# Performance work log

Hardware: AMD Instinct MI355X
Metric: run time of the kernel (lower is better)

The kernel has to match this reference:

```python
import jax, jax.numpy as jnp
import numpy as np

B, C, L = 8, 512, 2048
D = C // 8  # qk projection dim


def setup_inputs() -> dict:
    key = jax.random.key(0)
    ks = jax.random.split(key, 7)
    s = 0.02
    return {
        "x": jax.random.normal(ks[0], (B, C, L), dtype=jnp.float32),
        "data_mask": jnp.zeros((B, L, L), dtype=bool),
        "Wq": jax.random.normal(ks[1], (D, C), dtype=jnp.float32) * s,
        "bq": jnp.zeros((D,), dtype=jnp.float32),
        "Wk": jax.random.normal(ks[2], (D, C), dtype=jnp.float32) * s,
        "bk": jnp.zeros((D,), dtype=jnp.float32),
        "Wv": jax.random.normal(ks[3], (C, C), dtype=jnp.float32) * s,
        "bv": jnp.zeros((C,), dtype=jnp.float32),
    }


def reference(x, data_mask, Wq, bq, Wk, bk, Wv, bv):
    # Conv1d(kernel_size=1) == pointwise linear over channel dim.
    Lx = x.shape[-1]
    q = jnp.einsum("dc,bcl->bld", Wq, x) + bq              # (B, L, D)  == query_conv(x).permute(0,2,1)
    k = jnp.einsum("dc,bcl->bdl", Wk, x) + bk[:, None]     # (B, D, L)
    energy = jnp.einsum("bld,bdm->blm", q, k)              # (B, L, L)
    causal = jnp.triu(jnp.ones((Lx, Lx), dtype=bool), k=1)  # strictly-upper = masked
    mask = causal[None, :, :] | data_mask
    energy = jnp.where(mask, -jnp.inf, energy)
    attention = jax.nn.softmax(energy, axis=-1)            # (B, L, L)
    v = jnp.einsum("oc,bcl->bol", Wv, x) + bv[:, None]     # (B, C, L)
    # out = bmm(proj_value, attention^T): out[b,c,m] = sum_l v[b,c,l] * attention[b,m,l]
    out = jnp.einsum("bcl,bml->bcm", v, attention)         # (B, C, L)
    return out, attention
```

## Files before the change

### kernel.cpp

```cpp
#include <hip/hip_runtime.h>
#include <cstddef>
#include <math.h>

#define B_ 8
#define C_ 512
#define L_ 2048
#define D_ 64

typedef __bf16 bf16x8 __attribute__((ext_vector_type(8)));
typedef __bf16 bf16x4 __attribute__((ext_vector_type(4)));
typedef float f32x4 __attribute__((ext_vector_type(4)));

#define MFMA16 __builtin_amdgcn_mfma_f32_16x16x32_bf16

__device__ __forceinline__ void async_lds16(const void* g, void* l) {
  __builtin_amdgcn_global_load_lds(
      (const __attribute__((address_space(1))) void*)g,
      (__attribute__((address_space(3))) void*)l, 16, 0, 0);
}

__global__ __launch_bounds__(256) void transpose_cvt(const float* __restrict__ x,
                                                     __bf16* __restrict__ xT) {
  __shared__ float t[32][33];
  const int b = blockIdx.z;
  const int l0 = blockIdx.x * 32, c0 = blockIdx.y * 32;
  const int tx = threadIdx.x & 31, ty = threadIdx.x >> 5;
  const float* xb = x + (size_t)b * C_ * L_;
#pragma unroll
  for (int r = 0; r < 4; ++r)
    t[ty + r * 8][tx] = xb[(size_t)(c0 + ty + r * 8) * L_ + l0 + tx];
  __syncthreads();
  __bf16* xTb = xT + (size_t)b * L_ * C_;
#pragma unroll
  for (int r = 0; r < 4; ++r)
    xTb[(size_t)(l0 + ty + r * 8) * C_ + c0 + tx] = (__bf16)t[tx][ty + r * 8];
}

__global__ __launch_bounds__(256) void cvt_bf16(const float* __restrict__ in,
                                                __bf16* __restrict__ out, int n4) {
  const int i = blockIdx.x * 256 + threadIdx.x;
  if (i < n4) {
    float4 v = ((const float4*)in)[i];
    bf16x4 h = {(__bf16)v.x, (__bf16)v.y, (__bf16)v.z, (__bf16)v.w};
    ((bf16x4*)out)[i] = h;
  }
}

__global__ __launch_bounds__(256) void prep_qk(
    const float* __restrict__ Wq, const float* __restrict__ Wk,
    const float* __restrict__ bq, const float* __restrict__ bk,
    __bf16* __restrict__ Wqk, float* __restrict__ bqk) {
  const int i = blockIdx.x * 256 + threadIdx.x;
  const int half = 64 * 512 / 4;
  const float* src = (i < half) ? Wq : Wk;
  const int j = (i < half) ? i : i - half;
  float4 v = ((const float4*)src)[j];
  bf16x4 h = {(__bf16)v.x, (__bf16)v.y, (__bf16)v.z, (__bf16)v.w};
  ((bf16x4*)Wqk)[i] = h;
  if (blockIdx.x == 0 && threadIdx.x < 128)
    bqk[threadIdx.x] =
        threadIdx.x < 64 ? bq[threadIdx.x] : bk[threadIdx.x - 64];
}

template <int QK_MODE>
__global__ __launch_bounds__(256) void gemm_bt_mfma(
    const __bf16* __restrict__ A, const __bf16* __restrict__ B,
    const float* __restrict__ bias, __bf16* __restrict__ C0,
    __bf16* __restrict__ C1, int N, int K, int lda, int ldb, size_t strideA,
    size_t strideB, size_t strideC) {
  __shared__ __align__(16) __bf16 Ash[128 * 32];
  __shared__ __align__(16) __bf16 Bsh[128 * 32];
  const int b = blockIdx.z;
  const int m0 = blockIdx.x * 128;
  const int n0 = blockIdx.y * 128;
  const int tid = threadIdx.x;
  const int w = tid >> 6, lane = tid & 63;
  const int wm = (w & 1) * 64, wn = (w >> 1) * 64;
  const int lm = lane & 15, q8 = lane >> 4;
  const int srow = lane >> 2;
  const int sk8 = (lane & 3) ^ ((lane >> 3) & 3);

  const __bf16* Ab = A + strideA * b;
  const __bf16* Bb = B + strideB * b;
  f32x4 acc[4][4] = {};

  for (int k0 = 0; k0 < K; k0 += 32) {
#pragma unroll
    for (int t = 0; t < 2; ++t) {
      const int rb = (t * 4 + w) * 16;
      async_lds16(Ab + (size_t)(m0 + rb + srow) * lda + k0 + sk8 * 8,
                  &Ash[rb * 32]);
      async_lds16(Bb + (size_t)(n0 + rb + srow) * ldb + k0 + sk8 * 8,
                  &Bsh[rb * 32]);
    }
    __syncthreads();
    const int swz = (q8 ^ ((lm >> 1) & 3)) * 8;
    bf16x8 afr[4], bfr[4];
#pragma unroll
    for (int i = 0; i < 4; ++i) {
      afr[i] = *(const bf16x8*)&Ash[(wm + i * 16 + lm) * 32 + swz];
      bfr[i] = *(const bf16x8*)&Bsh[(wn + i * 16 + lm) * 32 + swz];
    }
#pragma unroll
    for (int i = 0; i < 4; ++i)
#pragma unroll
      for (int j = 0; j < 4; ++j)
        acc[i][j] = MFMA16(afr[i], bfr[j], acc[i][j], 0, 0, 0);
    __syncthreads();
  }

#pragma unroll
  for (int i = 0; i < 4; ++i) {
#pragma unroll
    for (int j = 0; j < 4; ++j) {
      const int ng = n0 + wn + j * 16 + lm;
      const int mgb = wm + i * 16 + q8 * 4;
      if (QK_MODE) {
        bf16x4 h;
#pragma unroll
        for (int r = 0; r < 4; ++r) h[r] = (__bf16)(acc[i][j][r] + bias[mgb + r]);
        if (mgb < 64)
          *(bf16x4*)&C0[((size_t)b * L_ + ng) * 64 + mgb] = h;
        else
          *(bf16x4*)&C1[((size_t)b * L_ + ng) * 64 + mgb - 64] = h;
      } else {
#pragma unroll
        for (int r = 0; r < 4; ++r) {
          const int mg = m0 + mgb + r;
          C0[strideC * b + (size_t)mg * N + ng] =
              (__bf16)(acc[i][j][r] + bias[mg]);
        }
      }
    }
  }
}

__global__ __launch_bounds__(256) void attn_fused(
    const __bf16* __restrict__ q, const __bf16* __restrict__ k,
    const __bf16* __restrict__ v, const unsigned char* __restrict__ mask,
    float* __restrict__ att, float* __restrict__ out) {
  __shared__ __align__(16) __bf16 qs[32 * 64];
  __shared__ __align__(16) __bf16 ks[2][128 * 64];
  __shared__ __align__(16) unsigned char msk[2][32 * 128];
  __shared__ __align__(16) __bf16 Ps[32 * 136];
  __shared__ float sums[4][32];
  __shared__ float invs[32];
  const int b = blockIdx.y;
  const int s = (b < 4) ? (int)blockIdx.x : 63 - (int)blockIdx.x;
  const int r0 = s * 32;
  const int T = (r0 + 31) / 128 + 1;
  const int tid = threadIdx.x;
  const int w = tid >> 6, lane = tid & 63;
  const int lm = lane & 15, q8 = lane >> 4;
  const __bf16* qb = q + (size_t)b * L_ * D_;
  const __bf16* kb = k + (size_t)b * L_ * D_;
  const __bf16* vb = v + (size_t)b * C_ * L_;
  const int krow = lane >> 3;
  const int kk8 = (lane & 7) ^ ((lane >> 3) & 7);

  bf16x8 af[2][2];
  float inv[2][4];
  f32x4 accO[2][8] = {};

  for (int pass = 0; pass < 2; ++pass) {
    __syncthreads();
    if (pass == 0)
      async_lds16(qb + (size_t)r0 * D_ + tid * 8, &qs[w * 512]);
#pragma unroll
    for (int r = 0; r < 4; ++r)
      async_lds16(kb + (size_t)(r * 32 + w * 8 + krow) * 64 + kk8 * 8,
                  &ks[0][(r * 32 + w * 8) * 64]);
    async_lds16(mask + (size_t)((size_t)b * L_ + r0 + w * 8 + krow) * L_ +
                    (lane & 7) * 16,
                &msk[0][w * 1024]);

    float rsum[2][4] = {};
    for (int t = 0; t < T; ++t) {
      const int t0 = t * 128;
      const int buf = t & 1;
      __syncthreads();
      if (pass == 0 && t == 0) {
#pragma unroll
        for (int i = 0; i < 2; ++i)
#pragma unroll
          for (int kk = 0; kk < 2; ++kk)
            af[i][kk] =
                *(const bf16x8*)&qs[(i * 16 + lm) * 64 + kk * 32 + q8 * 8];
      }
      if (t + 1 < T) {
        const int nt0 = t0 + 128, nb = (t + 1) & 1;
#pragma unroll
        for (int r = 0; r < 4; ++r)
          async_lds16(kb + (size_t)(nt0 + r * 32 + w * 8 + krow) * 64 + kk8 * 8,
                      &ks[nb][(r * 32 + w * 8) * 64]);
        async_lds16(mask + (size_t)((size_t)b * L_ + r0 + w * 8 + krow) * L_ +
                        nt0 + (lane & 7) * 16,
                    &msk[nb][w * 1024]);
      }
      f32x4 acc[2][2] = {};
#pragma unroll
      for (int kk = 0; kk < 2; ++kk) {
#pragma unroll
        for (int j = 0; j < 2; ++j) {
          const int n = w * 32 + j * 16 + lm;
          const int k8i = kk * 4 + q8;
          bf16x8 bf =
              *(const bf16x8*)&ks[buf][n * 64 + ((k8i ^ (n & 7)) * 8)];
#pragma unroll
          for (int i = 0; i < 2; ++i)
            acc[i][j] = MFMA16(af[i][kk], bf, acc[i][j], 0, 0, 0);
        }
      }
#pragma unroll
      for (int i = 0; i < 2; ++i)
#pragma unroll
        for (int j = 0; j < 2; ++j)
#pragma unroll
          for (int r = 0; r < 4; ++r) {
            const int lr = i * 16 + q8 * 4 + r;
            const int mcol = w * 32 + j * 16 + lm;
            const int l = r0 + lr, m = t0 + mcol;
            const bool ok = (m <= l) && (msk[buf][lr * 128 + mcol] == 0);
            const float p = ok ? __expf(acc[i][j][r]) : 0.f;
            if (pass == 0) {
              rsum[i][r] += p;
            } else {
              att[((size_t)b * L_ + l) * L_ + m] = p * inv[i][r];
              Ps[lr * 136 + mcol] = (__bf16)p;
            }
          }
      if (pass == 1) {
        __syncthreads();
#pragma unroll
        for (int kk = 0; kk < 4; ++kk) {
          bf16x8 pa[2];
#pragma unroll
          for (int i = 0; i < 2; ++i)
            pa[i] = *(const bf16x8*)&Ps[(i * 16 + lm) * 136 + kk * 32 + q8 * 8];
#pragma unroll
          for (int cf = 0; cf < 8; ++cf) {
            const int c = w * 128 + cf * 16 + lm;
            bf16x8 bv =
                *(const bf16x8*)(vb + (size_t)c * L_ + t0 + kk * 32 + q8 * 8);
#pragma unroll
            for (int i = 0; i < 2; ++i)
              accO[i][cf] = MFMA16(pa[i], bv, accO[i][cf], 0, 0, 0);
          }
        }
      }
    }
    if (pass == 0) {
#pragma unroll
      for (int i = 0; i < 2; ++i)
#pragma unroll
        for (int r = 0; r < 4; ++r) {
          float vv = rsum[i][r];
          vv += __shfl_xor(vv, 1);
          vv += __shfl_xor(vv, 2);
          vv += __shfl_xor(vv, 4);
          vv += __shfl_xor(vv, 8);
          if (lm == 0) sums[w][i * 16 + q8 * 4 + r] = vv;
        }
      __syncthreads();
      if (tid < 32)
        invs[tid] =
            1.f / (sums[0][tid] + sums[1][tid] + sums[2][tid] + sums[3][tid]);
      __syncthreads();
#pragma unroll
      for (int i = 0; i < 2; ++i)
#pragma unroll
        for (int r = 0; r < 4; ++r) inv[i][r] = invs[i * 16 + q8 * 4 + r];
    }
  }

#pragma unroll
  for (int i = 0; i < 2; ++i)
#pragma unroll
    for (int cf = 0; cf < 8; ++cf) {
      const int c = w * 128 + cf * 16 + lm;
      float4 o;
      o.x = accO[i][cf][0] * inv[i][0];
      o.y = accO[i][cf][1] * inv[i][1];
      o.z = accO[i][cf][2] * inv[i][2];
      o.w = accO[i][cf][3] * inv[i][3];
      *(float4*)(out + ((size_t)b * C_ + c) * L_ + r0 + i * 16 + q8 * 4) = o;
    }

  const float4 z4 = {0.f, 0.f, 0.f, 0.f};
  for (int rr = 0; rr < 32; ++rr) {
    float* arow = att + ((size_t)b * L_ + r0 + rr) * L_;
    for (int c = T * 128 + tid * 4; c < L_; c += 1024) *(float4*)&arow[c] = z4;
  }
}

extern "C" void kernel_launch(void* const* d_in, const int* in_sizes, int n_in,
                              void* d_out, int out_size, void* d_ws,
                              size_t ws_size, hipStream_t stream) {
  const float* x = (const float*)d_in[0];
  const unsigned char* dmask = (const unsigned char*)d_in[1];
  const float* Wq = (const float*)d_in[2];
  const float* bq = (const float*)d_in[3];
  const float* Wk = (const float*)d_in[4];
  const float* bk = (const float*)d_in[5];
  const float* Wv = (const float*)d_in[6];
  const float* bv = (const float*)d_in[7];

  float* out = (float*)d_out;
  float* att = out + (size_t)B_ * C_ * L_;

  __bf16* qh = (__bf16*)d_ws;
  __bf16* kh = qh + (size_t)B_ * L_ * D_;
  __bf16* xTh = kh + (size_t)B_ * L_ * D_;
  __bf16* Wvh = xTh + (size_t)B_ * L_ * C_;
  __bf16* vh = Wvh + (size_t)C_ * C_;
  __bf16* Wqk = vh + (size_t)B_ * C_ * L_;
  float* bqk = (float*)(Wqk + (size_t)128 * C_);

  dim3 blk(256);
  transpose_cvt<<<dim3(L_ / 32, C_ / 32, B_), blk, 0, stream>>>(x, xTh);
  cvt_bf16<<<dim3(C_ * C_ / 4 / 256), blk, 0, stream>>>(Wv, Wvh, C_ * C_ / 4);
  prep_qk<<<dim3(64), blk, 0, stream>>>(Wq, Wk, bq, bk, Wqk, bqk);
  gemm_bt_mfma<1><<<dim3(1, L_ / 128, B_), blk, 0, stream>>>(
      Wqk, xTh, bqk, qh, kh, L_, C_, C_, C_, 0, (size_t)L_ * C_, 0);
  gemm_bt_mfma<0><<<dim3(C_ / 128, L_ / 128, B_), blk, 0, stream>>>(
      Wvh, xTh, bv, vh, nullptr, L_, C_, C_, C_, 0, (size_t)L_ * C_,
      (size_t)C_ * L_);
  attn_fused<<<dim3(64, B_), blk, 0, stream>>>(qh, kh, vh, dmask, att, out);
}
```

Measured before the change: 417.4 us.

## Split softmax row-sum pass into separate kernel and fuse QKV projection GEMMs

The row-sum pass of the two-pass softmax moves out of the attention kernel into its own row_sums kernel, which writes inverse sums to workspace reused from the xT buffer. The attention kernel then does a single pass that writes attention and accumulates P·V. The Q/K and V weight conversions and GEMMs are also merged into one prep kernel and one 5-row-block GEMM launch, cutting launch count and letting the QK and V work share a grid. The extra kernel reloads Q/K/mask and adds a global round trip for the sums, but the attention kernel's per-block serial work is roughly halved.

```diff
diff --git a/kernel.cpp b/kernel.cpp
--- a/kernel.cpp
+++ b/kernel.cpp
@@ -36,38 +36,36 @@
     xTb[(size_t)(l0 + ty + r * 8) * C_ + c0 + tx] = (__bf16)t[tx][ty + r * 8];
 }
 
-__global__ __launch_bounds__(256) void cvt_bf16(const float* __restrict__ in,
-                                                __bf16* __restrict__ out, int n4) {
+__global__ __launch_bounds__(256) void prep_qkv(
+    const float* __restrict__ Wq, const float* __restrict__ Wk,
+    const float* __restrict__ Wv, const float* __restrict__ bq,
+    const float* __restrict__ bk, const float* __restrict__ bv,
+    __bf16* __restrict__ W, float* __restrict__ bias) {
   const int i = blockIdx.x * 256 + threadIdx.x;
-  if (i < n4) {
-    float4 v = ((const float4*)in)[i];
-    bf16x4 h = {(__bf16)v.x, (__bf16)v.y, (__bf16)v.z, (__bf16)v.w};
-    ((bf16x4*)out)[i] = h;
-  }
-}
-
-__global__ __launch_bounds__(256) void prep_qk(
-    const float* __restrict__ Wq, const float* __restrict__ Wk,
-    const float* __restrict__ bq, const float* __restrict__ bk,
-    __bf16* __restrict__ Wqk, float* __restrict__ bqk) {
-  const int i = blockIdx.x * 256 + threadIdx.x;
-  const int half = 64 * 512 / 4;
-  const float* src = (i < half) ? Wq : Wk;
-  const int j = (i < half) ? i : i - half;
+  const int rq = 64 * 512 / 4;
+  const int rk = 128 * 512 / 4;
+  const float* src;
+  int j;
+  if (i < rq) {
+    src = Wq; j = i;
+  } else if (i < rk) {
+    src = Wk; j = i - rq;
+  } else {
+    src = Wv; j = i - rk;
+  }
   float4 v = ((const float4*)src)[j];
   bf16x4 h = {(__bf16)v.x, (__bf16)v.y, (__bf16)v.z, (__bf16)v.w};
-  ((bf16x4*)Wqk)[i] = h;
-  if (blockIdx.x == 0 && threadIdx.x < 128)
-    bqk[threadIdx.x] =
-        threadIdx.x < 64 ? bq[threadIdx.x] : bk[threadIdx.x - 64];
-}
-
-template <int QK_MODE>
-__global__ __launch_bounds__(256) void gemm_bt_mfma(
-    const __bf16* __restrict__ A, const __bf16* __restrict__ B,
-    const float* __restrict__ bias, __bf16* __restrict__ C0,
-    __bf16* __restrict__ C1, int N, int K, int lda, int ldb, size_t strideA,
-    size_t strideB, size_t strideC) {
+  ((bf16x4*)W)[i] = h;
+  if (blockIdx.x == 0) {
+    for (int t = threadIdx.x; t < 640; t += 256)
+      bias[t] = t < 64 ? bq[t] : (t < 128 ? bk[t - 64] : bv[t - 128]);
+  }
+}
+
+__global__ __launch_bounds__(256) void gemm_qkv(
+    const __bf16* __restrict__ A, const __bf16* __restrict__ Bm,
+    const float* __restrict__ bias, __bf16* __restrict__ qh,
+    __bf16* __restrict__ kh, __bf16* __restrict__ vh) {
   __shared__ __align__(16) __bf16 Ash[128 * 32];
   __shared__ __align__(16) __bf16 Bsh[128 * 32];
   const int b = blockIdx.z;
@@ -80,17 +78,16 @@
   const int srow = lane >> 2;
   const int sk8 = (lane & 3) ^ ((lane >> 3) & 3);
 
-  const __bf16* Ab = A + strideA * b;
-  const __bf16* Bb = B + strideB * b;
+  const __bf16* Bb = Bm + (size_t)b * L_ * C_;
   f32x4 acc[4][4] = {};
 
-  for (int k0 = 0; k0 < K; k0 += 32) {
+  for (int k0 = 0; k0 < C_; k0 += 32) {
 #pragma unroll
     for (int t = 0; t < 2; ++t) {
       const int rb = (t * 4 + w) * 16;
-      async_lds16(Ab + (size_t)(m0 + rb + srow) * lda + k0 + sk8 * 8,
+      async_lds16(A + (size_t)(m0 + rb + srow) * C_ + k0 + sk8 * 8,
                   &Ash[rb * 32]);
-      async_lds16(Bb + (size_t)(n0 + rb + srow) * ldb + k0 + sk8 * 8,
+      async_lds16(Bb + (size_t)(n0 + rb + srow) * C_ + k0 + sk8 * 8,
                   &Bsh[rb * 32]);
     }
     __syncthreads();
@@ -114,37 +111,126 @@
 #pragma unroll
     for (int j = 0; j < 4; ++j) {
       const int ng = n0 + wn + j * 16 + lm;
-      const int mgb = wm + i * 16 + q8 * 4;
-      if (QK_MODE) {
+      const int mg = m0 + wm + i * 16 + q8 * 4;
+      if (mg < 128) {
         bf16x4 h;
 #pragma unroll
-        for (int r = 0; r < 4; ++r) h[r] = (__bf16)(acc[i][j][r] + bias[mgb + r]);
-        if (mgb < 64)
-          *(bf16x4*)&C0[((size_t)b * L_ + ng) * 64 + mgb] = h;
+        for (int r = 0; r < 4; ++r) h[r] = (__bf16)(acc[i][j][r] + bias[mg + r]);
+        if (mg < 64)
+          *(bf16x4*)&qh[((size_t)b * L_ + ng) * 64 + mg] = h;
         else
-          *(bf16x4*)&C1[((size_t)b * L_ + ng) * 64 + mgb - 64] = h;
+          *(bf16x4*)&kh[((size_t)b * L_ + ng) * 64 + mg - 64] = h;
       } else {
 #pragma unroll
+        for (int r = 0; r < 4; ++r)
+          vh[((size_t)b * C_ + mg - 128 + r) * L_ + ng] =
+              (__bf16)(acc[i][j][r] + bias[mg + r]);
+      }
+    }
+  }
+}
+
+__global__ __launch_bounds__(256) void row_sums(
+    const __bf16* __restrict__ q, const __bf16* __restrict__ k,
+    const unsigned char* __restrict__ mask, float* __restrict__ sinv) {
+  __shared__ __align__(16) __bf16 qs[32 * 64];
+  __shared__ __align__(16) __bf16 ks[2][128 * 64];
+  __shared__ __align__(16) unsigned char msk[2][32 * 128];
+  __shared__ float sums[4][32];
+  const int b = blockIdx.y;
+  const int s = (b < 4) ? (int)blockIdx.x : 63 - (int)blockIdx.x;
+  const int r0 = s * 32;
+  const int T = (r0 + 31) / 128 + 1;
+  const int tid = threadIdx.x;
+  const int w = tid >> 6, lane = tid & 63;
+  const int lm = lane & 15, q8 = lane >> 4;
+  const __bf16* qb = q + (size_t)b * L_ * D_;
+  const __bf16* kb = k + (size_t)b * L_ * D_;
+  const int krow = lane >> 3;
+  const int kk8 = (lane & 7) ^ ((lane >> 3) & 7);
+
+  async_lds16(qb + (size_t)r0 * D_ + tid * 8, &qs[w * 512]);
+#pragma unroll
+  for (int r = 0; r < 4; ++r)
+    async_lds16(kb + (size_t)(r * 32 + w * 8 + krow) * 64 + kk8 * 8,
+                &ks[0][(r * 32 + w * 8) * 64]);
+  async_lds16(mask + ((size_t)b * L_ + r0 + w * 8 + krow) * L_ + (lane & 7) * 16,
+              &msk[0][w * 1024]);
+
+  bf16x8 af[2][2];
+  float rsum[2][4] = {};
+  for (int t = 0; t < T; ++t) {
+    const int t0 = t * 128, buf = t & 1;
+    __syncthreads();
+    if (t == 0) {
+#pragma unroll
+      for (int i = 0; i < 2; ++i)
+#pragma unroll
+        for (int kk = 0; kk < 2; ++kk)
+          af[i][kk] = *(const bf16x8*)&qs[(i * 16 + lm) * 64 + kk * 32 + q8 * 8];
+    }
+    if (t + 1 < T) {
+      const int nt0 = t0 + 128, nb = (t + 1) & 1;
+#pragma unroll
+      for (int r = 0; r < 4; ++r)
+        async_lds16(kb + (size_t)(nt0 + r * 32 + w * 8 + krow) * 64 + kk8 * 8,
+                    &ks[nb][(r * 32 + w * 8) * 64]);
+      async_lds16(mask + ((size_t)b * L_ + r0 + w * 8 + krow) * L_ + nt0 +
+                      (lane & 7) * 16,
+                  &msk[nb][w * 1024]);
+    }
+    f32x4 acc[2][2] = {};
+#pragma unroll
+    for (int kk = 0; kk < 2; ++kk) {
+#pragma unroll
+      for (int j = 0; j < 2; ++j) {
+        const int n = w * 32 + j * 16 + lm;
+        const int k8i = kk * 4 + q8;
+        bf16x8 bf = *(const bf16x8*)&ks[buf][n * 64 + ((k8i ^ (n & 7)) * 8)];
+#pragma unroll
+        for (int i = 0; i < 2; ++i)
+          acc[i][j] = MFMA16(af[i][kk], bf, acc[i][j], 0, 0, 0);
+      }
+    }
+#pragma unroll
+    for (int i = 0; i < 2; ++i)
+#pragma unroll
+      for (int j = 0; j < 2; ++j)
+#pragma unroll
         for (int r = 0; r < 4; ++r) {
-          const int mg = m0 + mgb + r;
-          C0[strideC * b + (size_t)mg * N + ng] =
-              (__bf16)(acc[i][j][r] + bias[mg]);
+          const int lr = i * 16 + q8 * 4 + r;
+          const int mcol = w * 32 + j * 16 + lm;
+          const int l = r0 + lr, m = t0 + mcol;
+          const bool ok = (m <= l) && (msk[buf][lr * 128 + mcol] == 0);
+          rsum[i][r] += ok ? __expf(acc[i][j][r]) : 0.f;
         }
-      }
-    }
-  }
+  }
+#pragma unroll
+  for (int i = 0; i < 2; ++i)
+#pragma unroll
+    for (int r = 0; r < 4; ++r) {
+      float vv = rsum[i][r];
+      vv += __shfl_xor(vv, 1);
+      vv += __shfl_xor(vv, 2);
+      vv += __shfl_xor(vv, 4);
+      vv += __shfl_xor(vv, 8);
+      if (lm == 0) sums[w][i * 16 + q8 * 4 + r] = vv;
+    }
+  __syncthreads();
+  if (tid < 32)
+    sinv[(size_t)b * L_ + r0 + tid] =
+        1.f / (sums[0][tid] + sums[1][tid] + sums[2][tid] + sums[3][tid]);
 }
 
 __global__ __launch_bounds__(256) void attn_fused(
     const __bf16* __restrict__ q, const __bf16* __restrict__ k,
     const __bf16* __restrict__ v, const unsigned char* __restrict__ mask,
-    float* __restrict__ att, float* __restrict__ out) {
+    const float* __restrict__ sinv, float* __restrict__ att,
+    float* __restrict__ out) {
   __shared__ __align__(16) __bf16 qs[32 * 64];
   __shared__ __align__(16) __bf16 ks[2][128 * 64];
   __shared__ __align__(16) unsigned char msk[2][32 * 128];
   __shared__ __align__(16) __bf16 Ps[32 * 136];
-  __shared__ float sums[4][32];
-  __shared__ float invs[32];
   const int b = blockIdx.y;
   const int s = (b < 4) ? (int)blockIdx.x : 63 - (int)blockIdx.x;
   const int r0 = s * 32;
@@ -158,118 +244,87 @@
   const int krow = lane >> 3;
   const int kk8 = (lane & 7) ^ ((lane >> 3) & 7);
 
+  float inv[2][4];
+#pragma unroll
+  for (int i = 0; i < 2; ++i)
+#pragma unroll
+    for (int r = 0; r < 4; ++r)
+      inv[i][r] = sinv[(size_t)b * L_ + r0 + i * 16 + q8 * 4 + r];
+
   bf16x8 af[2][2];
-  float inv[2][4];
   f32x4 accO[2][8] = {};
 
-  for (int pass = 0; pass < 2; ++pass) {
-    __syncthreads();
-    if (pass == 0)
-      async_lds16(qb + (size_t)r0 * D_ + tid * 8, &qs[w * 512]);
-#pragma unroll
-    for (int r = 0; r < 4; ++r)
-      async_lds16(kb + (size_t)(r * 32 + w * 8 + krow) * 64 + kk8 * 8,
-                  &ks[0][(r * 32 + w * 8) * 64]);
-    async_lds16(mask + (size_t)((size_t)b * L_ + r0 + w * 8 + krow) * L_ +
-                    (lane & 7) * 16,
-                &msk[0][w * 1024]);
-
-    float rsum[2][4] = {};
-    for (int t = 0; t < T; ++t) {
-      const int t0 = t * 128;
-      const int buf = t & 1;
-      __syncthreads();
-      if (pass == 0 && t == 0) {
+  async_lds16(qb + (size_t)r0 * D_ + tid * 8, &qs[w * 512]);
+#pragma unroll
+  for (int r = 0; r < 4; ++r)
+    async_lds16(kb + (size_t)(r * 32 + w * 8 + krow) * 64 + kk8 * 8,
+                &ks[0][(r * 32 + w * 8) * 64]);
+  async_lds16(mask + ((size_t)b * L_ + r0 + w * 8 + krow) * L_ + (lane & 7) * 16,
+              &msk[0][w * 1024]);
+
+  for (int t = 0; t < T; ++t) {
+    const int t0 = t * 128, buf = t & 1;
+    __syncthreads();
+    if (t == 0) {
+#pragma unroll
+      for (int i = 0; i < 2; ++i)
+#pragma unroll
+        for (int kk = 0; kk < 2; ++kk)
+          af[i][kk] = *(const bf16x8*)&qs[(i * 16 + lm) * 64 + kk * 32 + q8 * 8];
+    }
+    if (t + 1 < T) {
+      const int nt0 = t0 + 128, nb = (t + 1) & 1;
+#pragma unroll
+      for (int r = 0; r < 4; ++r)
+        async_lds16(kb + (size_t)(nt0 + r * 32 + w * 8 + krow) * 64 + kk8 * 8,
+                    &ks[nb][(r * 32 + w * 8) * 64]);
+      async_lds16(mask + ((size_t)b * L_ + r0 + w * 8 + krow) * L_ + nt0 +
+                      (lane & 7) * 16,
+                  &msk[nb][w * 1024]);
+    }
+    f32x4 acc[2][2] = {};
+#pragma unroll
+    for (int kk = 0; kk < 2; ++kk) {
+#pragma unroll
+      for (int j = 0; j < 2; ++j) {
+        const int n = w * 32 + j * 16 + lm;
+        const int k8i = kk * 4 + q8;
+        bf16x8 bf = *(const bf16x8*)&ks[buf][n * 64 + ((k8i ^ (n & 7)) * 8)];
 #pragma unroll
         for (int i = 0; i < 2; ++i)
-#pragma unroll
-          for (int kk = 0; kk < 2; ++kk)
-            af[i][kk] =
-                *(const bf16x8*)&qs[(i * 16 + lm) * 64 + kk * 32 + q8 * 8];
+          acc[i][j] = MFMA16(af[i][kk], bf, acc[i][j], 0, 0, 0);
       }
-      if (t + 1 < T) {
-        const int nt0 = t0 + 128, nb = (t + 1) & 1;
-#pragma unroll
-        for (int r = 0; r < 4; ++r)
-          async_lds16(kb + (size_t)(nt0 + r * 32 + w * 8 + krow) * 64 + kk8 * 8,
-                      &ks[nb][(r * 32 + w * 8) * 64]);
-        async_lds16(mask + (size_t)((size_t)b * L_ + r0 + w * 8 + krow) * L_ +
-                        nt0 + (lane & 7) * 16,
-                    &msk[nb][w * 1024]);
+    }
+#pragma unroll
+    for (int i = 0; i < 2; ++i)
+#pragma unroll
+      for (int j = 0; j < 2; ++j)
+#pragma unroll
+        for (int r = 0; r < 4; ++r) {
+          const int lr = i * 16 + q8 * 4 + r;
+          const int mcol = w * 32 + j * 16 + lm;
+          const int l = r0 + lr, m = t0 + mcol;
+          const bool ok = (m <= l) && (msk[buf][lr * 128 + mcol] == 0);
+          const float p = ok ? __expf(acc[i][j][r]) : 0.f;
+          att[((size_t)b * L_ + l) * L_ + m] = p * inv[i][r];
+          Ps[lr * 136 + mcol] = (__bf16)p;
+        }
+    __syncthreads();
+#pragma unroll
+    for (int kk = 0; kk < 4; ++kk) {
+      bf16x8 pa[2];
+#pragma unroll
+      for (int i = 0; i < 2; ++i)
+        pa[i] = *(const bf16x8*)&Ps[(i * 16 + lm) * 136 + kk * 32 + q8 * 8];
+#pragma unroll
+      for (int cf = 0; cf < 8; ++cf) {
+        const int c = w * 128 + cf * 16 + lm;
+        bf16x8 bv =
+            *(const bf16x8*)(vb + (size_t)c * L_ + t0 + kk * 32 + q8 * 8);
+#pragma unroll
+        for (int i = 0; i < 2; ++i)
+          accO[i][cf] = MFMA16(pa[i], bv, accO[i][cf], 0, 0, 0);
       }
-      f32x4 acc[2][2] = {};
-#pragma unroll
-      for (int kk = 0; kk < 2; ++kk) {
-#pragma unroll
-        for (int j = 0; j < 2; ++j) {
-          const int n = w * 32 + j * 16 + lm;
-          const int k8i = kk * 4 + q8;
-          bf16x8 bf =
-              *(const bf16x8*)&ks[buf][n * 64 + ((k8i ^ (n & 7)) * 8)];
-#pragma unroll
-          for (int i = 0; i < 2; ++i)
-            acc[i][j] = MFMA16(af[i][kk], bf, acc[i][j], 0, 0, 0);
-        }
-      }
-#pragma unroll
-      for (int i = 0; i < 2; ++i)
-#pragma unroll
-        for (int j = 0; j < 2; ++j)
-#pragma unroll
-          for (int r = 0; r < 4; ++r) {
-            const int lr = i * 16 + q8 * 4 + r;
-            const int mcol = w * 32 + j * 16 + lm;
-            const int l = r0 + lr, m = t0 + mcol;
-            const bool ok = (m <= l) && (msk[buf][lr * 128 + mcol] == 0);
-            const float p = ok ? __expf(acc[i][j][r]) : 0.f;
-            if (pass == 0) {
-              rsum[i][r] += p;
-            } else {
-              att[((size_t)b * L_ + l) * L_ + m] = p * inv[i][r];
-              Ps[lr * 136 + mcol] = (__bf16)p;
-            }
-          }
-      if (pass == 1) {
-        __syncthreads();
-#pragma unroll
-        for (int kk = 0; kk < 4; ++kk) {
-          bf16x8 pa[2];
-#pragma unroll
-          for (int i = 0; i < 2; ++i)
-            pa[i] = *(const bf16x8*)&Ps[(i * 16 + lm) * 136 + kk * 32 + q8 * 8];
-#pragma unroll
-          for (int cf = 0; cf < 8; ++cf) {
-            const int c = w * 128 + cf * 16 + lm;
-            bf16x8 bv =
-                *(const bf16x8*)(vb + (size_t)c * L_ + t0 + kk * 32 + q8 * 8);
-#pragma unroll
-            for (int i = 0; i < 2; ++i)
-              accO[i][cf] = MFMA16(pa[i], bv, accO[i][cf], 0, 0, 0);
-          }
-        }
-      }
-    }
-    if (pass == 0) {
-#pragma unroll
-      for (int i = 0; i < 2; ++i)
-#pragma unroll
-        for (int r = 0; r < 4; ++r) {
-          float vv = rsum[i][r];
-          vv += __shfl_xor(vv, 1);
-          vv += __shfl_xor(vv, 2);
-          vv += __shfl_xor(vv, 4);
-          vv += __shfl_xor(vv, 8);
-          if (lm == 0) sums[w][i * 16 + q8 * 4 + r] = vv;
-        }
-      __syncthreads();
-      if (tid < 32)
-        invs[tid] =
-            1.f / (sums[0][tid] + sums[1][tid] + sums[2][tid] + sums[3][tid]);
-      __syncthreads();
-#pragma unroll
-      for (int i = 0; i < 2; ++i)
-#pragma unroll
-        for (int r = 0; r < 4; ++r) inv[i][r] = invs[i * 16 + q8 * 4 + r];
     }
   }
 
@@ -311,19 +366,17 @@
   __bf16* qh = (__bf16*)d_ws;
   __bf16* kh = qh + (size_t)B_ * L_ * D_;
   __bf16* xTh = kh + (size_t)B_ * L_ * D_;
-  __bf16* Wvh = xTh + (size_t)B_ * L_ * C_;
-  __bf16* vh = Wvh + (size_t)C_ * C_;
-  __bf16* Wqk = vh + (size_t)B_ * C_ * L_;
-  float* bqk = (float*)(Wqk + (size_t)128 * C_);
+  __bf16* vh = xTh + (size_t)B_ * L_ * C_;
+  __bf16* Wqkv = vh + (size_t)B_ * C_ * L_;
+  float* bqkv = (float*)(Wqkv + (size_t)640 * C_);
+  float* sinv = (float*)xTh;
 
   dim3 blk(256);
   transpose_cvt<<<dim3(L_ / 32, C_ / 32, B_), blk, 0, stream>>>(x, xTh);
-  cvt_bf16<<<dim3(C_ * C_ / 4 / 256), blk, 0, stream>>>(Wv, Wvh, C_ * C_ / 4);
-  prep_qk<<<dim3(64), blk, 0, stream>>>(Wq, Wk, bq, bk, Wqk, bqk);
-  gemm_bt_mfma<1><<<dim3(1, L_ / 128, B_), blk, 0, stream>>>(
-      Wqk, xTh, bqk, qh, kh, L_, C_, C_, C_, 0, (size_t)L_ * C_, 0);
-  gemm_bt_mfma<0><<<dim3(C_ / 128, L_ / 128, B_), blk, 0, stream>>>(
-      Wvh, xTh, bv, vh, nullptr, L_, C_, C_, C_, 0, (size_t)L_ * C_,
-      (size_t)C_ * L_);
-  attn_fused<<<dim3(64, B_), blk, 0, stream>>>(qh, kh, vh, dmask, att, out);
-}
+  prep_qkv<<<dim3(320), blk, 0, stream>>>(Wq, Wk, Wv, bq, bk, bv, Wqkv, bqkv);
+  gemm_qkv<<<dim3(5, L_ / 128, B_), blk, 0, stream>>>(Wqkv, xTh, bqkv, qh, kh,
+                                                      vh);
+  row_sums<<<dim3(64, B_), blk, 0, stream>>>(qh, kh, dmask, sinv);
+  attn_fused<<<dim3(64, B_), blk, 0, stream>>>(qh, kh, vh, dmask, sinv, att,
+                                               out);
+}
```

New measurement: 417.3 us. No clear change (-0.0%).
